# Optimization experiments

Hardware: AMD Instinct MI355X
Metric: run time of the kernel (lower is better)

Reference implementation:

```python
import jax, jax.numpy as jnp
import numpy as np

B, N, D = 2, 2048, 512
H, VD = 8, 64  # v_dim = hid_dim / n_head


def setup_inputs() -> dict:
    key = jax.random.key(0)
    k1, k2, k3, k4 = jax.random.split(key, 4)
    inputs = jax.random.normal(k1, (B, N, D), dtype=jnp.float32)
    # lecun_normal: std = 1/sqrt(fan_in) with fan_in = D
    s = 1.0 / np.sqrt(D)
    q_w = jax.random.normal(k2, (H, D, VD), dtype=jnp.float32) * s
    k_w = jax.random.normal(k3, (H, D, VD), dtype=jnp.float32) * s
    v_w = jax.random.normal(k4, (H, D, VD), dtype=jnp.float32) * s
    return {"inputs": inputs, "q_w": q_w, "k_w": k_w, "v_w": v_w}


def reference(inputs, q_w, k_w, v_w):
    # QKV projections: [B,N,D] x [H,D,VD] -> [B,H,N,VD]
    q = jnp.einsum('bnj,hjk->bhnk', inputs, q_w)
    k = jnp.einsum('bnj,hjk->bhnk', inputs, k_w)
    v = jnp.einsum('bnj,hjk->bhnk', inputs, v_w)
    scale = 1.0 / jnp.sqrt(jnp.asarray(VD, dtype=q.dtype))
    scores = jnp.einsum('bhik,bhjk->bhij', q, k) * scale  # [B,H,N,N]
    att = jax.nn.softmax(scores, axis=-1)
    out = jnp.einsum('bhnj,bhjd->bhnd', att, v)  # [B,H,N,VD]
    out = jnp.transpose(out, (0, 2, 1, 3)).reshape(inputs.shape[0], -1, H * VD)  # [B,N,hid_dim]
    # keras GELU default is exact (non-approximate)
    return jax.nn.gelu(out, approximate=False)
```

## Files before the change

### kernel.cpp

```cpp
#include <hip/hip_runtime.h>
#include <hip/hip_bf16.h>
#include <math.h>

#define BB 2
#define NN 2048
#define DD 512
#define HH 8
#define VD 64

typedef _Float16 half8 __attribute__((ext_vector_type(8)));
typedef _Float16 half4 __attribute__((ext_vector_type(4)));
typedef __fp16 fp16x2 __attribute__((ext_vector_type(2)));
typedef float f32x4 __attribute__((ext_vector_type(4)));

#define GLDS16(gp, lp) __builtin_amdgcn_global_load_lds( \
    (const __attribute__((address_space(1))) void*)(gp), \
    (__attribute__((address_space(3))) void*)(lp), 16, 0, 0)

__device__ __forceinline__ float fexp2(float x) {
#if __has_builtin(__builtin_amdgcn_exp2f)
    return __builtin_amdgcn_exp2f(x);
#else
    return exp2f(x);
#endif
}

__device__ __forceinline__ void stage8(const _Float16* gsrc, size_t ldg, int r0,
                                       _Float16* lbase, int lane) {
    int r8 = lane >> 3;
    int ce = ((lane & 7) ^ r8) << 3;
    const _Float16* g = gsrc + (size_t)(r0 + r8) * ldg + ce;
    GLDS16(g, lbase);
}

__device__ __forceinline__ half8 frag_ld(const _Float16* tile, int row, int cb) {
    int off = row * 128 + (cb ^ ((row & 7) << 4));
    return *(const half8*)((const char*)tile + off);
}

__device__ __forceinline__ float gelu_exact(float v) {
    return 0.5f * v * (1.f + erff(v * 0.70710678118654752f));
}

__global__ __launch_bounds__(256) void prep_kernel(
    const float* __restrict__ x,
    const float* __restrict__ qw, const float* __restrict__ kw,
    const float* __restrict__ vw,
    _Float16* __restrict__ wt, _Float16* __restrict__ xh)
{
    __shared__ float ls[64][65];
    const int t = threadIdx.x;
    const int bid = blockIdx.x;
    if (bid < 192) {
        const int kc = bid & 7, h = (bid >> 3) & 7, ty = bid >> 6;
        const float* src = (ty == 0) ? qw : (ty == 1) ? kw : vw;
#pragma unroll
        for (int j = 0; j < 4; ++j) {
            int idx = t + 256 * j;
            int k = idx >> 4, o4 = idx & 15;
            float4 v = *(const float4*)(src + ((size_t)(h * DD + kc * 64 + k) * VD + o4 * 4));
            ls[k][o4 * 4 + 0] = v.x; ls[k][o4 * 4 + 1] = v.y;
            ls[k][o4 * 4 + 2] = v.z; ls[k][o4 * 4 + 3] = v.w;
        }
        __syncthreads();
#pragma unroll
        for (int j = 0; j < 4; ++j) {
            int idx = t + 256 * j;
            int o = idx >> 4, k4 = idx & 15;
            half4 hv;
#pragma unroll
            for (int i = 0; i < 4; ++i) hv[i] = (_Float16)ls[k4 * 4 + i][o];
            *(half4*)(wt + ((size_t)(ty * HH + h) * VD + o) * DD + kc * 64 + k4 * 4) = hv;
        }
    } else {
        size_t idx = ((size_t)(bid - 192) * 256 + t) * 8;
        float4 a = *(const float4*)(x + idx);
        float4 b = *(const float4*)(x + idx + 4);
        half8 hv;
        hv[0] = (_Float16)a.x; hv[1] = (_Float16)a.y;
        hv[2] = (_Float16)a.z; hv[3] = (_Float16)a.w;
        hv[4] = (_Float16)b.x; hv[5] = (_Float16)b.y;
        hv[6] = (_Float16)b.z; hv[7] = (_Float16)b.w;
        *(half8*)(xh + idx) = hv;
    }
}

__global__ __launch_bounds__(256) void qkv_proj_kernel(
    const _Float16* __restrict__ xh,
    const _Float16* __restrict__ wt,
    _Float16* __restrict__ qsp,
    _Float16* __restrict__ kbp,
    _Float16* __restrict__ vtp)
{
    __shared__ __align__(16) _Float16 xls[2][4096];
    __shared__ __align__(16) _Float16 wls[2][12288];
    const int t = threadIdx.x;
    const int wave = t >> 6, lane = t & 63;
    const int lq = lane & 15, g = lane >> 4;
    const int bid = blockIdx.x;
    const int h = bid & 7;
    const int m0 = (bid >> 3) * 64;
    const int rbase = 32 * (wave >> 1);
    const int cbase = 96 * (wave & 1);

    f32x4 acc[2][6];
#pragma unroll
    for (int a = 0; a < 2; ++a)
#pragma unroll
        for (int c = 0; c < 6; ++c) acc[a][c] = (f32x4){0.f, 0.f, 0.f, 0.f};

    auto stage = [&](int buf, int ks) {
#pragma unroll
        for (int j = 0; j < 2; ++j) {
            int i = wave * 2 + j;
            stage8(xh + (size_t)m0 * DD + ks * 64, DD, i * 8, &xls[buf][i * 512], lane);
        }
#pragma unroll
        for (int j = 0; j < 6; ++j) {
            int i = wave * 6 + j;
            int ty = i >> 3;
            int ol = (i & 7) * 8;
            stage8(wt + ((size_t)(ty * HH + h) * VD + ol) * DD + ks * 64, DD, 0,
                   &wls[buf][i * 512], lane);
        }
    };

    stage(0, 0);
    __syncthreads();
    int buf = 0;
    for (int ks = 0; ks < 8; ++ks) {
        if (ks < 7) stage(buf ^ 1, ks + 1);
        half8 af[2][2];
        half8 bf[6][2];
#pragma unroll
        for (int amt = 0; amt < 2; ++amt) {
            af[amt][0] = frag_ld(xls[buf], rbase + amt * 16 + lq, 16 * g);
            af[amt][1] = frag_ld(xls[buf], rbase + amt * 16 + lq, 64 + 16 * g);
        }
#pragma unroll
        for (int ct = 0; ct < 6; ++ct) {
            int wr = cbase + ct * 16 + lq;
            bf[ct][0] = frag_ld(wls[buf], wr, 16 * g);
            bf[ct][1] = frag_ld(wls[buf], wr, 64 + 16 * g);
        }
#pragma unroll
        for (int ct = 0; ct < 6; ++ct) {
#pragma unroll
            for (int amt = 0; amt < 2; ++amt) {
                acc[amt][ct] = __builtin_amdgcn_mfma_f32_16x16x32_f16(af[amt][0], bf[ct][0], acc[amt][ct], 0, 0, 0);
                acc[amt][ct] = __builtin_amdgcn_mfma_f32_16x16x32_f16(af[amt][1], bf[ct][1], acc[amt][ct], 0, 0, 0);
            }
        }
        __syncthreads();
        buf ^= 1;
    }

#pragma unroll
    for (int ct = 0; ct < 6; ++ct) {
        int gcol = cbase + ct * 16 + lq;
        int ty = gcol >> 6, o = gcol & 63;
#pragma unroll
        for (int amt = 0; amt < 2; ++amt) {
#pragma unroll
            for (int i = 0; i < 4; ++i) {
                int ng = m0 + rbase + amt * 16 + 4 * g + i;
                int b = ng >> 11, nb = ng & (NN - 1);
                size_t bh = (size_t)(b * HH + h);
                float v = acc[amt][ct][i];
                if (ty == 0)      qsp[(bh * NN + nb) * VD + o] = (_Float16)(v * 0.18033688011112042f);
                else if (ty == 1) kbp[(bh * NN + nb) * VD + o] = (_Float16)v;
                else              vtp[(bh * VD + o) * NN + nb] = (_Float16)v;
            }
        }
    }
}

__global__ __launch_bounds__(256) void attn_kernel(
    const _Float16* __restrict__ qs,
    const _Float16* __restrict__ kb,
    const _Float16* __restrict__ vt,
    float* __restrict__ out)
{
    constexpr int NITER = NN / 64;
    __shared__ __align__(16) _Float16 kls[3][4096];
    __shared__ __align__(16) _Float16 vls[3][4096];
    const int t = threadIdx.x;
    const int wave = t >> 6, lane = t & 63;
    const int lq = lane & 15, g = lane >> 4;
    const int bid = blockIdx.x;
    const int xcd = bid & 7;
    const int bh = xcd * 2 + ((bid >> 3) & 1);
    const int qt = bid >> 4;
    const int qbase = qt * 128 + wave * 32;

    half8 qf[2][2];
#pragma unroll
    for (int qh = 0; qh < 2; ++qh) {
        const _Float16* qp = qs + ((size_t)bh * NN + qbase + qh * 16 + lq) * VD + 8 * g;
        qf[qh][0] = *(const half8*)qp;
        qf[qh][1] = *(const half8*)(qp + 32);
    }

    const int r8 = lane >> 3;
    const int dchunk = (lane & 7) ^ r8;
    const int krow0 = 16 * (r8 >> 2) + 4 * wave + (r8 & 3);
    const _Float16* kgA = kb + (size_t)bh * NN * VD + (size_t)krow0 * VD + dchunk * 8;
    const int kvst = 16 * (dchunk & 3) + 8 * (dchunk >> 2);
    const _Float16* vgA = vt + (size_t)bh * VD * NN + (size_t)(wave * 16 + r8) * NN + kvst;

    f32x4 oacc[2][4];
#pragma unroll
    for (int qh = 0; qh < 2; ++qh)
#pragma unroll
        for (int mt = 0; mt < 4; ++mt) oacc[qh][mt] = (f32x4){0.f, 0.f, 0.f, 0.f};
    float lsum[2] = {0.f, 0.f};

    auto stagekv = [&](_Float16* kd, _Float16* vd, int itn) {
        const _Float16* kp = kgA + (size_t)itn * (64 * VD);
        GLDS16(kp,           kd + wave * 1024);
        GLDS16(kp + 32 * VD, kd + wave * 1024 + 512);
        const _Float16* vp = vgA + itn * 64;
        GLDS16(vp,           vd + wave * 1024);
        GLDS16(vp + 8 * NN,  vd + wave * 1024 + 512);
    };

    _Float16 *k0 = &kls[0][0], *k1 = &kls[1][0], *k2 = &kls[2][0];
    _Float16 *v0 = &vls[0][0], *v1 = &vls[1][0], *v2 = &vls[2][0];
    stagekv(k0, v0, 0);
    stagekv(k1, v1, 1);
    stagekv(k2, v2, 2);

    union PU { fp16x2 h2[4]; half8 h8; };

    for (int j = 0; j < NITER; ++j) {
        if (j < NITER - 2)       asm volatile("s_waitcnt vmcnt(8)" ::: "memory");
        else if (j == NITER - 2) asm volatile("s_waitcnt vmcnt(4)" ::: "memory");
        else                     asm volatile("s_waitcnt vmcnt(0)" ::: "memory");
        __builtin_amdgcn_s_barrier();
        half8 kf[4][2], vf[2][4];
#pragma unroll
        for (int mt = 0; mt < 4; ++mt) {
            kf[mt][0] = frag_ld(k0, mt * 16 + lq, 16 * g);
            kf[mt][1] = frag_ld(k0, mt * 16 + lq, 64 + 16 * g);
        }
#pragma unroll
        for (int kc = 0; kc < 2; ++kc)
#pragma unroll
            for (int mt = 0; mt < 4; ++mt)
                vf[kc][mt] = frag_ld(v0, mt * 16 + lq, kc * 64 + 16 * g);
        asm volatile("s_waitcnt lgkmcnt(0)" ::: "memory");
        __builtin_amdgcn_sched_barrier(0);
        __builtin_amdgcn_s_barrier();
        if (j + 3 < NITER) stagekv(k0, v0, j + 3);
        f32x4 sv[2][4];
        __builtin_amdgcn_s_setprio(1);
#pragma unroll
        for (int mt = 0; mt < 4; ++mt) {
#pragma unroll
            for (int qh = 0; qh < 2; ++qh) {
                sv[qh][mt] = (f32x4){0.f, 0.f, 0.f, 0.f};
                sv[qh][mt] = __builtin_amdgcn_mfma_f32_16x16x32_f16(kf[mt][0], qf[qh][0], sv[qh][mt], 0, 0, 0);
                sv[qh][mt] = __builtin_amdgcn_mfma_f32_16x16x32_f16(kf[mt][1], qf[qh][1], sv[qh][mt], 0, 0, 0);
            }
        }
        __builtin_amdgcn_s_setprio(0);
        PU pu[2][2];
#pragma unroll
        for (int qh = 0; qh < 2; ++qh) {
#pragma unroll
            for (int mt = 0; mt < 4; ++mt) {
                float p0 = fexp2(sv[qh][mt][0]);
                float p1 = fexp2(sv[qh][mt][1]);
                float p2 = fexp2(sv[qh][mt][2]);
                float p3 = fexp2(sv[qh][mt][3]);
                lsum[qh] += (p0 + p1) + (p2 + p3);
                pu[qh][mt >> 1].h2[(mt & 1) * 2 + 0] = __builtin_amdgcn_cvt_pkrtz(p0, p1);
                pu[qh][mt >> 1].h2[(mt & 1) * 2 + 1] = __builtin_amdgcn_cvt_pkrtz(p2, p3);
            }
        }
        __builtin_amdgcn_s_setprio(1);
#pragma unroll
        for (int kc = 0; kc < 2; ++kc) {
#pragma unroll
            for (int mt = 0; mt < 4; ++mt) {
                oacc[0][mt] = __builtin_amdgcn_mfma_f32_16x16x32_f16(vf[kc][mt], pu[0][kc].h8, oacc[0][mt], 0, 0, 0);
                oacc[1][mt] = __builtin_amdgcn_mfma_f32_16x16x32_f16(vf[kc][mt], pu[1][kc].h8, oacc[1][mt], 0, 0, 0);
            }
        }
        __builtin_amdgcn_s_setprio(0);
        _Float16* tk = k0; k0 = k1; k1 = k2; k2 = tk;
        _Float16* tv = v0; v0 = v1; v1 = v2; v2 = tv;
    }

    const int b = bh >> 3, h = bh & 7;
#pragma unroll
    for (int qh = 0; qh < 2; ++qh) {
        float l = lsum[qh];
        l += __shfl_xor(l, 16, 64);
        l += __shfl_xor(l, 32, 64);
        float inv = 1.f / l;
        float* op = out + ((size_t)b * NN + qbase + qh * 16 + lq) * (HH * VD) + h * VD;
#pragma unroll
        for (int mt = 0; mt < 4; ++mt) {
            float4 r;
            r.x = gelu_exact(oacc[qh][mt][0] * inv);
            r.y = gelu_exact(oacc[qh][mt][1] * inv);
            r.z = gelu_exact(oacc[qh][mt][2] * inv);
            r.w = gelu_exact(oacc[qh][mt][3] * inv);
            *(float4*)(op + mt * 16 + 4 * g) = r;
        }
    }
}

extern "C" void kernel_launch(void* const* d_in, const int* in_sizes, int n_in,
                              void* d_out, int out_size, void* d_ws, size_t ws_size,
                              hipStream_t stream)
{
    const float* x  = (const float*)d_in[0];
    const float* qw = (const float*)d_in[1];
    const float* kw = (const float*)d_in[2];
    const float* vw = (const float*)d_in[3];
    float* out = (float*)d_out;

    _Float16* wt  = (_Float16*)d_ws;
    _Float16* xhp = wt  + 786432;
    _Float16* qsp = xhp + 2097152;
    _Float16* kbp = qsp + 2097152;
    _Float16* vtp = kbp + 2097152;

    hipLaunchKernelGGL(prep_kernel, dim3(192 + 1024), dim3(256), 0, stream,
                       x, qw, kw, vw, wt, xhp);
    hipLaunchKernelGGL(qkv_proj_kernel, dim3(512), dim3(256), 0, stream,
                       xhp, wt, qsp, kbp, vtp);
    hipLaunchKernelGGL(attn_kernel, dim3(256), dim3(256), 0, stream,
                       qsp, kbp, vtp, out);
}
```

Measured before the change: 55.52 us.

## Halve attention query tile to double grid, deepen projection pipeline

The attention kernel now gives each wave 16 query rows instead of 32, and the grid doubles to 512 blocks, so more workgroups cover the 256 CUs. This costs twice the K/V traffic per query. The projection GEMM switches from a synchronous double buffer to a two-ahead prefetch with explicit vmcnt waits, barriers and raised priority around the MFMAs, aiming to overlap global loads with compute. The block-index mapping (qt = bid>>4) still covers all tiles with the larger grid.

```diff
diff --git a/kernel.cpp b/kernel.cpp
--- a/kernel.cpp
+++ b/kernel.cpp
@@ -126,10 +126,12 @@
     };
 
     stage(0, 0);
-    __syncthreads();
-    int buf = 0;
+    stage(1, 1);
     for (int ks = 0; ks < 8; ++ks) {
-        if (ks < 7) stage(buf ^ 1, ks + 1);
+        const int buf = ks & 1;
+        if (ks < 7) asm volatile("s_waitcnt vmcnt(8)" ::: "memory");
+        else        asm volatile("s_waitcnt vmcnt(0)" ::: "memory");
+        __builtin_amdgcn_s_barrier();
         half8 af[2][2];
         half8 bf[6][2];
 #pragma unroll
@@ -143,6 +145,11 @@
             bf[ct][0] = frag_ld(wls[buf], wr, 16 * g);
             bf[ct][1] = frag_ld(wls[buf], wr, 64 + 16 * g);
         }
+        asm volatile("s_waitcnt lgkmcnt(0)" ::: "memory");
+        __builtin_amdgcn_sched_barrier(0);
+        __builtin_amdgcn_s_barrier();
+        if (ks + 2 < 8) stage(buf, ks + 2);
+        __builtin_amdgcn_s_setprio(1);
 #pragma unroll
         for (int ct = 0; ct < 6; ++ct) {
 #pragma unroll
@@ -151,8 +158,7 @@
                 acc[amt][ct] = __builtin_amdgcn_mfma_f32_16x16x32_f16(af[amt][1], bf[ct][1], acc[amt][ct], 0, 0, 0);
             }
         }
-        __syncthreads();
-        buf ^= 1;
+        __builtin_amdgcn_s_setprio(0);
     }
 
 #pragma unroll
@@ -191,14 +197,13 @@
     const int xcd = bid & 7;
     const int bh = xcd * 2 + ((bid >> 3) & 1);
     const int qt = bid >> 4;
-    const int qbase = qt * 128 + wave * 32;
-
-    half8 qf[2][2];
-#pragma unroll
-    for (int qh = 0; qh < 2; ++qh) {
-        const _Float16* qp = qs + ((size_t)bh * NN + qbase + qh * 16 + lq) * VD + 8 * g;
-        qf[qh][0] = *(const half8*)qp;
-        qf[qh][1] = *(const half8*)(qp + 32);
+    const int qbase = qt * 64 + wave * 16;
+
+    half8 qf[2];
+    {
+        const _Float16* qp = qs + ((size_t)bh * NN + qbase + lq) * VD + 8 * g;
+        qf[0] = *(const half8*)qp;
+        qf[1] = *(const half8*)(qp + 32);
     }
 
     const int r8 = lane >> 3;
@@ -208,12 +213,10 @@
     const int kvst = 16 * (dchunk & 3) + 8 * (dchunk >> 2);
     const _Float16* vgA = vt + (size_t)bh * VD * NN + (size_t)(wave * 16 + r8) * NN + kvst;
 
-    f32x4 oacc[2][4];
-#pragma unroll
-    for (int qh = 0; qh < 2; ++qh)
-#pragma unroll
-        for (int mt = 0; mt < 4; ++mt) oacc[qh][mt] = (f32x4){0.f, 0.f, 0.f, 0.f};
-    float lsum[2] = {0.f, 0.f};
+    f32x4 oacc[4];
+#pragma unroll
+    for (int mt = 0; mt < 4; ++mt) oacc[mt] = (f32x4){0.f, 0.f, 0.f, 0.f};
+    float lsum = 0.f;
 
     auto stagekv = [&](_Float16* kd, _Float16* vd, int itn) {
         const _Float16* kp = kgA + (size_t)itn * (64 * VD);
@@ -252,63 +255,51 @@
         __builtin_amdgcn_sched_barrier(0);
         __builtin_amdgcn_s_barrier();
         if (j + 3 < NITER) stagekv(k0, v0, j + 3);
-        f32x4 sv[2][4];
+        f32x4 sv[4];
         __builtin_amdgcn_s_setprio(1);
 #pragma unroll
         for (int mt = 0; mt < 4; ++mt) {
-#pragma unroll
-            for (int qh = 0; qh < 2; ++qh) {
-                sv[qh][mt] = (f32x4){0.f, 0.f, 0.f, 0.f};
-                sv[qh][mt] = __builtin_amdgcn_mfma_f32_16x16x32_f16(kf[mt][0], qf[qh][0], sv[qh][mt], 0, 0, 0);
-                sv[qh][mt] = __builtin_amdgcn_mfma_f32_16x16x32_f16(kf[mt][1], qf[qh][1], sv[qh][mt], 0, 0, 0);
-            }
+            sv[mt] = (f32x4){0.f, 0.f, 0.f, 0.f};
+            sv[mt] = __builtin_amdgcn_mfma_f32_16x16x32_f16(kf[mt][0], qf[0], sv[mt], 0, 0, 0);
+            sv[mt] = __builtin_amdgcn_mfma_f32_16x16x32_f16(kf[mt][1], qf[1], sv[mt], 0, 0, 0);
         }
         __builtin_amdgcn_s_setprio(0);
-        PU pu[2][2];
-#pragma unroll
-        for (int qh = 0; qh < 2; ++qh) {
-#pragma unroll
-            for (int mt = 0; mt < 4; ++mt) {
-                float p0 = fexp2(sv[qh][mt][0]);
-                float p1 = fexp2(sv[qh][mt][1]);
-                float p2 = fexp2(sv[qh][mt][2]);
-                float p3 = fexp2(sv[qh][mt][3]);
-                lsum[qh] += (p0 + p1) + (p2 + p3);
-                pu[qh][mt >> 1].h2[(mt & 1) * 2 + 0] = __builtin_amdgcn_cvt_pkrtz(p0, p1);
-                pu[qh][mt >> 1].h2[(mt & 1) * 2 + 1] = __builtin_amdgcn_cvt_pkrtz(p2, p3);
-            }
+        PU pu[2];
+#pragma unroll
+        for (int mt = 0; mt < 4; ++mt) {
+            float p0 = fexp2(sv[mt][0]);
+            float p1 = fexp2(sv[mt][1]);
+            float p2 = fexp2(sv[mt][2]);
+            float p3 = fexp2(sv[mt][3]);
+            lsum += (p0 + p1) + (p2 + p3);
+            pu[mt >> 1].h2[(mt & 1) * 2 + 0] = __builtin_amdgcn_cvt_pkrtz(p0, p1);
+            pu[mt >> 1].h2[(mt & 1) * 2 + 1] = __builtin_amdgcn_cvt_pkrtz(p2, p3);
         }
         __builtin_amdgcn_s_setprio(1);
 #pragma unroll
-        for (int kc = 0; kc < 2; ++kc) {
-#pragma unroll
-            for (int mt = 0; mt < 4; ++mt) {
-                oacc[0][mt] = __builtin_amdgcn_mfma_f32_16x16x32_f16(vf[kc][mt], pu[0][kc].h8, oacc[0][mt], 0, 0, 0);
-                oacc[1][mt] = __builtin_amdgcn_mfma_f32_16x16x32_f16(vf[kc][mt], pu[1][kc].h8, oacc[1][mt], 0, 0, 0);
-            }
-        }
+        for (int kc = 0; kc < 2; ++kc)
+#pragma unroll
+            for (int mt = 0; mt < 4; ++mt)
+                oacc[mt] = __builtin_amdgcn_mfma_f32_16x16x32_f16(vf[kc][mt], pu[kc].h8, oacc[mt], 0, 0, 0);
         __builtin_amdgcn_s_setprio(0);
         _Float16* tk = k0; k0 = k1; k1 = k2; k2 = tk;
         _Float16* tv = v0; v0 = v1; v1 = v2; v2 = tv;
     }
 
     const int b = bh >> 3, h = bh & 7;
-#pragma unroll
-    for (int qh = 0; qh < 2; ++qh) {
-        float l = lsum[qh];
-        l += __shfl_xor(l, 16, 64);
-        l += __shfl_xor(l, 32, 64);
-        float inv = 1.f / l;
-        float* op = out + ((size_t)b * NN + qbase + qh * 16 + lq) * (HH * VD) + h * VD;
-#pragma unroll
-        for (int mt = 0; mt < 4; ++mt) {
-            float4 r;
-            r.x = gelu_exact(oacc[qh][mt][0] * inv);
-            r.y = gelu_exact(oacc[qh][mt][1] * inv);
-            r.z = gelu_exact(oacc[qh][mt][2] * inv);
-            r.w = gelu_exact(oacc[qh][mt][3] * inv);
-            *(float4*)(op + mt * 16 + 4 * g) = r;
-        }
+    float l = lsum;
+    l += __shfl_xor(l, 16, 64);
+    l += __shfl_xor(l, 32, 64);
+    float inv = 1.f / l;
+    float* op = out + ((size_t)b * NN + qbase + lq) * (HH * VD) + h * VD;
+#pragma unroll
+    for (int mt = 0; mt < 4; ++mt) {
+        float4 r;
+        r.x = gelu_exact(oacc[mt][0] * inv);
+        r.y = gelu_exact(oacc[mt][1] * inv);
+        r.z = gelu_exact(oacc[mt][2] * inv);
+        r.w = gelu_exact(oacc[mt][3] * inv);
+        *(float4*)(op + mt * 16 + 4 * g) = r;
     }
 }
 
@@ -332,6 +323,6 @@
                        x, qw, kw, vw, wt, xhp);
     hipLaunchKernelGGL(qkv_proj_kernel, dim3(512), dim3(256), 0, stream,
                        xhp, wt, qsp, kbp, vtp);
-    hipLaunchKernelGGL(attn_kernel, dim3(256), dim3(256), 0, stream,
+    hipLaunchKernelGGL(attn_kernel, dim3(512), dim3(256), 0, stream,
                        qsp, kbp, vtp, out);
 }
```

Measured after the change: 52.97 us. 4.6% less time.
